# Optimization experiments

Measured on AMD Instinct MI355X. Metric: run time of the kernel, lower is better.

Reference implementation:

```python
import jax, jax.numpy as jnp
import numpy as np

B, N, F_IN, F_OUT = 1024, 16, 1024, 4096  # n_nodes=16 and n_heads=1 are structurally fixed by the module


def setup_inputs() -> dict:
    key = jax.random.key(0)
    ks = jax.random.split(key, 7)
    s1 = 1.0 / np.sqrt(F_IN)
    s2 = 1.0 / np.sqrt(F_IN * 16)
    return {
        "x": jax.random.normal(ks[0], (B, N, F_IN), jnp.float32),
        "matrix": jax.random.uniform(ks[1], (B, N, N), jnp.float32),
        "W1": jax.random.uniform(ks[2], (F_IN, F_IN), jnp.float32, -s1, s1),
        "b1": jax.random.uniform(ks[3], (F_IN,), jnp.float32, -s1, s1),
        "W_mlp": jax.random.uniform(ks[4], (F_OUT, F_IN * 16), jnp.float32, -s2, s2),
        "b_mlp": jax.random.uniform(ks[5], (F_OUT,), jnp.float32, -s2, s2),
        "a_param": jnp.float32(5.0),
    }


def _l2norm(v):
    # matches F.normalize(p=2, dim=-1, eps=1e-12)
    n = jnp.maximum(jnp.linalg.norm(v, axis=-1, keepdims=True), 1e-12)
    return v / n


def _forward(x, matrix, W1, b1, W_mlp, b_mlp, a_param):
    Bc, n, f = x.shape  # n_heads = 1, n_hidden = f
    wg = x @ W1.T + b1                                    # [B,n,f]
    gs = _l2norm(x)                                       # g_reshaped (H=1)
    gt = _l2norm(wg)                                      # g_transposed
    e = jnp.einsum('bik,bjk->bij', gs, gt)[..., None]     # [B,n,n,1] cosine scores
    eye = jnp.eye(n, dtype=x.dtype)[None, :, :, None]
    e = e * (1.0 + eye * a_param)                         # boost diagonal
    a_scores = e                                          # pre-softmax scores (used below)
    esm = jax.nn.softmax(e, axis=1)                       # softmax over dim=1
    m = matrix[..., None]                                 # [B,n,n,1]
    # MPUGAT message passing
    from_i = jnp.einsum('bitp,btkp->bikp', esm, m)        # [B,n,n,1]
    diag = jnp.einsum('bkkp->bkp', m)                     # diagonal of matrix
    from_j = esm * diag[:, None, :, :]                    # '...jkp,...kkp->...jkp'
    e2 = jnp.einsum('bikp,bjkp->bijp', from_i, from_j)    # [B,n,n,1]
    e2 = 0.5 * (e2 + jnp.transpose(e2, (0, 2, 1, 3)))
    # attention readout with PRE-softmax scores a_scores
    g = x.reshape(Bc, n, 1, f)                            # [B,n,H=1,f]
    attn = jnp.tanh(jnp.einsum('bjhf,bjih->bihf', g, a_scores))  # [B,n,1,f]
    out = attn.reshape(Bc, -1) @ W_mlp.T + b_mlp          # [B,F_OUT]
    out = jnp.broadcast_to(out[:, None, :], (Bc, 16, out.shape[-1]))  # repeat(1,16,1)
    return out, e2, m


def reference(x, matrix, W1, b1, W_mlp, b_mlp, a_param):
    return _forward(x, matrix, W1, b1, W_mlp, b_mlp, a_param)
```

## Files before the change

kernel.cpp:

```cpp
#include <hip/hip_runtime.h>
#include <math.h>

typedef short short8 __attribute__((ext_vector_type(8)));
typedef float f32x4 __attribute__((ext_vector_type(4)));
typedef unsigned short us4 __attribute__((ext_vector_type(4)));
typedef unsigned int u32x4 __attribute__((ext_vector_type(4)));
typedef unsigned short u16;
typedef unsigned int u32;

#define GAS __attribute__((address_space(1)))
#define LAS __attribute__((address_space(3)))

static __device__ __forceinline__ u16 f2bf(float f) {
    union { float f; u32 u; } v; v.f = f;
    u32 r = v.u + 0x7FFFu + ((v.u >> 16) & 1u);
    return (u16)(r >> 16);
}

static __device__ __forceinline__ u32 pk2(float a, float b) {
    return (u32)f2bf(a) | ((u32)f2bf(b) << 16);
}

static __device__ __forceinline__ u32 cvtpk(float lo, float hi) {
    u32 r;
    asm("v_cvt_pk_bf16_f32 %0, %1, %2" : "=v"(r) : "v"(lo), "v"(hi));
    return r;
}

static __device__ __forceinline__ float bf2f(u16 h) {
    union { u32 u; float f; } v; v.u = ((u32)h) << 16;
    return v.f;
}

static __device__ __forceinline__ float ftanh(float v) {
    float t = __expf(-2.0f * fabsf(v));
    float r = (1.0f - t) / (1.0f + t);
    return copysignf(r, v);
}

static __device__ __forceinline__ void gll16(const void* g, void* l) {
    __builtin_amdgcn_global_load_lds((const GAS void*)g, (LAS void*)l, 16, 0, 0);
}

__global__ __launch_bounds__(256) void k_cvt_x(const float* __restrict__ x,
                                               u16* __restrict__ xb,
                                               float* __restrict__ xinv,
                                               const float* __restrict__ W1,
                                               u16* __restrict__ w1b) {
    const int bid = blockIdx.x, t = threadIdx.x;
    if (bid >= 16384) {
        const size_t i = (size_t)(bid - 16384) * 256 + t;
        const f32x4 v = *(const f32x4*)(W1 + 4 * i);
        u32* dst = (u32*)(w1b + 4 * i);
        dst[0] = pk2(v.x, v.y); dst[1] = pk2(v.z, v.w);
        return;
    }
    const int row = bid;
    const f32x4 v = *(const f32x4*)(x + (size_t)row * 1024 + 4 * t);
    u32* dst = (u32*)(xb + (size_t)row * 1024 + 4 * t);
    dst[0] = pk2(v.x, v.y); dst[1] = pk2(v.z, v.w);
    float s = v.x * v.x + v.y * v.y + v.z * v.z + v.w * v.w;
#pragma unroll
    for (int off = 1; off < 64; off <<= 1) s += __shfl_xor(s, off, 64);
    __shared__ float red[4];
    if ((t & 63) == 0) red[t >> 6] = s;
    __syncthreads();
    if (t == 0)
        xinv[row] = 1.0f / fmaxf(sqrtf(red[0] + red[1] + red[2] + red[3]), 1e-12f);
}

#define MFMA16(a, b, c) __builtin_amdgcn_mfma_f32_16x16x32_bf16(a, b, c, 0, 0, 0)
#define SBAR() __builtin_amdgcn_s_barrier()
#define SCHED0() __builtin_amdgcn_sched_barrier(0)
#define PHFENCE() do { SBAR(); SCHED0(); } while (0)
#define VMW6 asm volatile("s_waitcnt vmcnt(6)" ::: "memory")
#define VMW4 asm volatile("s_waitcnt vmcnt(4)" ::: "memory")
#define VMW2 asm volatile("s_waitcnt vmcnt(2)" ::: "memory")
#define VMW0 asm volatile("s_waitcnt vmcnt(0)" ::: "memory")
#define VMW8L asm volatile("s_waitcnt vmcnt(8) lgkmcnt(0)" ::: "memory")
#define LGKML asm volatile("s_waitcnt lgkmcnt(0)" ::: "memory")
#define VMNOP do {} while (0)

#define DO_T1(I0, I1, I2, I3, W0, W1M, W2, W3)                                \
  do {                                                                        \
    short8 Af[4][2], Bf0[2][2], Bf1[2][2];                                    \
    _Pragma("unroll") for (int m = 0; m < 4; ++m) {                           \
      Af[m][0] = *(const short8*)(la + rpA[m] + sw0);                         \
      Af[m][1] = *(const short8*)(la + rpA[m] + sw1);                         \
    }                                                                         \
    _Pragma("unroll") for (int n = 0; n < 2; ++n) {                           \
      Bf0[n][0] = *(const short8*)(lb + rpB[n] + sw0);                        \
      Bf0[n][1] = *(const short8*)(lb + rpB[n] + sw1);                        \
    }                                                                         \
    if (I0) { gll16(AG + (saO00 + knxa), danext + ldst);                      \
              gll16(AG + (saO01 + knxa), danext + 4096 + ldst); }             \
    SBAR(); SCHED0();                                                         \
    __builtin_amdgcn_s_setprio(1);                                            \
    _Pragma("unroll") for (int k = 0; k < 2; ++k)                             \
      _Pragma("unroll") for (int m = 0; m < 4; ++m)                           \
        _Pragma("unroll") for (int n = 0; n < 2; ++n)                         \
          acc[m][n] = MFMA16(Af[m][k], Bf0[n][k], acc[m][n]);                 \
    __builtin_amdgcn_s_setprio(0); SCHED0(); W0; SBAR();                      \
    _Pragma("unroll") for (int n = 0; n < 2; ++n) {                           \
      Bf1[n][0] = *(const short8*)(lb + rpB[n + 2] + sw0);                    \
      Bf1[n][1] = *(const short8*)(lb + rpB[n + 2] + sw1);                    \
    }                                                                         \
    if (I1) { gll16(BG + (sbO10 + knxa), dbnext + 8192 + ldst);               \
              gll16(BG + (sbO11 + knxa), dbnext + 8192 + 4096 + ldst); }      \
    SBAR(); SCHED0();                                                         \
    __builtin_amdgcn_s_setprio(1);                                            \
    _Pragma("unroll") for (int k = 0; k < 2; ++k)                             \
      _Pragma("unroll") for (int m = 0; m < 4; ++m)                           \
        _Pragma("unroll") for (int n = 0; n < 2; ++n)                         \
          acc[m][n + 2] = MFMA16(Af[m][k], Bf1[n][k], acc[m][n + 2]);         \
    __builtin_amdgcn_s_setprio(0); SCHED0(); W1M; SBAR();                     \
    _Pragma("unroll") for (int m = 0; m < 4; ++m) {                           \
      Af[m][0] = *(const short8*)(la + rpA[m + 4] + sw0);                     \
      Af[m][1] = *(const short8*)(la + rpA[m + 4] + sw1);                     \
    }                                                                         \
    if (I2) { gll16(AG + (saO10 + knxa), danext + 8192 + ldst);               \
              gll16(AG + (saO11 + knxa), danext + 8192 + 4096 + ldst); }      \
    SBAR(); SCHED0();                                                         \
    __builtin_amdgcn_s_setprio(1);                                            \
    _Pragma("unroll") for (int k = 0; k < 2; ++k)                             \
      _Pragma("unroll") for (int m = 0; m < 4; ++m)                           \
        _Pragma("unroll") for (int n = 0; n < 2; ++n)                         \
          acc[m + 4][n] = MFMA16(Af[m][k], Bf0[n][k], acc[m + 4][n]);         \
    __builtin_amdgcn_s_setprio(0); SCHED0(); W2; SBAR();                      \
    if (I3) { gll16(BG + (sbO00 + knxb), lbw + ldst);                         \
              gll16(BG + (sbO01 + knxb), lbw + 4096 + ldst); }                \
    SBAR(); SCHED0();                                                         \
    __builtin_amdgcn_s_setprio(1);                                            \
    _Pragma("unroll") for (int k = 0; k < 2; ++k)                             \
      _Pragma("unroll") for (int m = 0; m < 4; ++m)                           \
        _Pragma("unroll") for (int n = 0; n < 2; ++n)                         \
          acc[m + 4][n + 2] = MFMA16(Af[m][k], Bf1[n][k], acc[m + 4][n + 2]); \
    __builtin_amdgcn_s_setprio(0); SCHED0(); W3; SBAR();                      \
  } while (0)

#define GEMM1_PROLOGUE()                                                      \
  do {                                                                        \
    gll16(AG + saO00, &LsA[0][0] + ldst);                                     \
    gll16(AG + saO01, &LsA[0][0] + 4096 + ldst);                              \
    gll16(BG + sbO00, &LsB[0][0] + ldst);                                     \
    gll16(BG + sbO01, &LsB[0][0] + 4096 + ldst);                              \
    gll16(BG + sbO10, &LsB[0][0] + 8192 + ldst);                              \
    gll16(BG + sbO11, &LsB[0][0] + 8192 + 4096 + ldst);                       \
    gll16(AG + saO10, &LsA[0][0] + 8192 + ldst);                              \
    gll16(AG + saO11, &LsA[0][0] + 8192 + 4096 + ldst);                       \
    gll16(BG + sbO00 + 64, &LsB[1][0] + ldst);                                \
    gll16(BG + sbO01 + 64, &LsB[1][0] + 4096 + ldst);                         \
    VMW6; SBAR();                                                             \
  } while (0)

#define GT2S(ISS, KNXA, KNXB, WAITX)                                          \
  do {                                                                        \
    short8 Af[4][2], Bf0[2][2], Bf1[2][2];                                    \
    _Pragma("unroll") for (int m = 0; m < 4; ++m) {                           \
      Af[m][0] = *(const short8*)(la + rpA[m] + sw0);                         \
      Af[m][1] = *(const short8*)(la + rpA[m] + sw1);                         \
    }                                                                         \
    _Pragma("unroll") for (int n = 0; n < 2; ++n) {                           \
      Bf0[n][0] = *(const short8*)(lb + rpB[n] + sw0);                        \
      Bf0[n][1] = *(const short8*)(lb + rpB[n] + sw1);                        \
    }                                                                         \
    if (ISS) { gll16(AG + (saO00 + (KNXA)), danext + ldst);                   \
               gll16(AG + (saO01 + (KNXA)), danext + 4096 + ldst); }          \
    PHFENCE();                                                                \
    __builtin_amdgcn_s_setprio(1);                                            \
    _Pragma("unroll") for (int k = 0; k < 2; ++k)                             \
      _Pragma("unroll") for (int m = 0; m < 4; ++m)                           \
        _Pragma("unroll") for (int n = 0; n < 2; ++n)                         \
          acc[m][n] = MFMA16(Af[m][k], Bf0[n][k], acc[m][n]);                 \
    __builtin_amdgcn_s_setprio(0); SCHED0(); SBAR();                          \
    _Pragma("unroll") for (int n = 0; n < 2; ++n) {                           \
      Bf1[n][0] = *(const short8*)(lb + rpB[n + 2] + sw0);                    \
      Bf1[n][1] = *(const short8*)(lb + rpB[n + 2] + sw1);                    \
    }                                                                         \
    if (ISS) { gll16(AG + (saO10 + (KNXA)), danext + 8192 + ldst);            \
               gll16(AG + (saO11 + (KNXA)), danext + 8192 + 4096 + ldst); }   \
    PHFENCE();                                                                \
    __builtin_amdgcn_s_setprio(1);                                            \
    _Pragma("unroll") for (int k = 0; k < 2; ++k)                             \
      _Pragma("unroll") for (int m = 0; m < 4; ++m)                           \
        _Pragma("unroll") for (int n = 0; n < 2; ++n)                         \
          acc[m][n + 2] = MFMA16(Af[m][k], Bf1[n][k], acc[m][n + 2]);         \
    __builtin_amdgcn_s_setprio(0); SCHED0(); SBAR();                          \
    _Pragma("unroll") for (int m = 0; m < 4; ++m) {                           \
      Af[m][0] = *(const short8*)(la + rpA[m + 4] + sw0);                     \
      Af[m][1] = *(const short8*)(la + rpA[m + 4] + sw1);                     \
    }                                                                         \
    PHFENCE();                                                                \
    __builtin_amdgcn_s_setprio(1);                                            \
    _Pragma("unroll") for (int k = 0; k < 2; ++k)                             \
      _Pragma("unroll") for (int m = 0; m < 4; ++m)                           \
        _Pragma("unroll") for (int n = 0; n < 2; ++n)                         \
          acc[m + 4][n] = MFMA16(Af[m][k], Bf0[n][k], acc[m + 4][n]);         \
    __builtin_amdgcn_s_setprio(0); SCHED0();                                  \
    if (ISS) {                                                                \
      _Pragma("unroll") for (int c = 0; c < 2; ++c) {                         \
        u32x4 wv;                                                             \
        wv.x = cvtpk(bn[2 * c].x, bn[2 * c].y);                               \
        wv.y = cvtpk(bn[2 * c].z, bn[2 * c].w);                               \
        wv.z = cvtpk(bn[2 * c + 1].x, bn[2 * c + 1].y);                       \
        wv.w = cvtpk(bn[2 * c + 1].z, bn[2 * c + 1].w);                       \
        *(u32x4*)(dbnext + c * 4096 + (tid << 3)) = wv;                       \
        bn[2 * c]     = *(const f32x4*)(BGf + bro[c] + (KNXB) + swsrc);       \
        bn[2 * c + 1] = *(const f32x4*)(BGf + bro[c] + (KNXB) + swsrc + 4);   \
      }                                                                       \
    }                                                                         \
    __builtin_amdgcn_s_setprio(1);                                            \
    _Pragma("unroll") for (int k = 0; k < 2; ++k)                             \
      _Pragma("unroll") for (int m = 0; m < 4; ++m)                           \
        _Pragma("unroll") for (int n = 0; n < 2; ++n)                         \
          acc[m + 4][n + 2] = MFMA16(Af[m][k], Bf1[n][k], acc[m + 4][n + 2]); \
    __builtin_amdgcn_s_setprio(0); SCHED0();                                  \
    if (ISS) {                                                                \
      _Pragma("unroll") for (int c = 2; c < 4; ++c) {                         \
        u32x4 wv;                                                             \
        wv.x = cvtpk(bn[2 * c].x, bn[2 * c].y);                               \
        wv.y = cvtpk(bn[2 * c].z, bn[2 * c].w);                               \
        wv.z = cvtpk(bn[2 * c + 1].x, bn[2 * c + 1].y);                       \
        wv.w = cvtpk(bn[2 * c + 1].z, bn[2 * c + 1].w);                       \
        *(u32x4*)(dbnext + c * 4096 + (tid << 3)) = wv;                       \
        bn[2 * c]     = *(const f32x4*)(BGf + bro[c] + (KNXB) + swsrc);       \
        bn[2 * c + 1] = *(const f32x4*)(BGf + bro[c] + (KNXB) + swsrc + 4);   \
      }                                                                       \
    }                                                                         \
    WAITX; SBAR();                                                            \
  } while (0)

__global__ __launch_bounds__(512, 2) void k_gemm1_8ph(const u16* __restrict__ AG,
                                                      const u16* __restrict__ BG,
                                                      const float* __restrict__ bias,
                                                      u16* __restrict__ C,
                                                      float* __restrict__ wgn2) {
    __shared__ __align__(16) u16 LsA[2][16384];
    __shared__ __align__(16) u16 LsB[2][16384];
    const int K = 1024, NT = 16;
    const int lin = blockIdx.x;
    const int w = (lin & 7) * 32 + (lin >> 3);
    const int n0 = (w & 3) * 256;
    const int m0 = (w >> 2) * 256;

    const int tid = threadIdx.x, wave = tid >> 6, lane = tid & 63;
    const int lr = lane & 15, kq = lane >> 4;
    const int wr = wave >> 2, wc = wave & 3;

    const int trow = tid >> 3;
    const u32 swsrc = (u32)(((tid & 7) ^ (trow & 7)) * 8);
    const u32 saO00 = (u32)(m0 + 0 + trow) * (u32)K + swsrc;
    const u32 saO01 = (u32)(m0 + 128 + trow) * (u32)K + swsrc;
    const u32 saO10 = (u32)(m0 + 64 + trow) * (u32)K + swsrc;
    const u32 saO11 = (u32)(m0 + 192 + trow) * (u32)K + swsrc;
    const int q0 = trow, q1 = 64 + trow;
    const u32 sbO00 = (u32)(n0 + (q0 >> 5) * 64 + (q0 & 31)) * (u32)K + swsrc;
    const u32 sbO01 = (u32)(n0 + (q1 >> 5) * 64 + (q1 & 31)) * (u32)K + swsrc;
    const u32 sbO10 = (u32)(n0 + (q0 >> 5) * 64 + 32 + (q0 & 31)) * (u32)K + swsrc;
    const u32 sbO11 = (u32)(n0 + (q1 >> 5) * 64 + 32 + (q1 & 31)) * (u32)K + swsrc;
    const u32 ldst = (u32)wave * 512;

    int rpA[8], rpB[4];
#pragma unroll
    for (int mf = 0; mf < 8; ++mf)
        rpA[mf] = ((mf >> 2) * 128 + wr * 64 + (mf & 3) * 16 + lr) << 6;
#pragma unroll
    for (int nf = 0; nf < 4; ++nf)
        rpB[nf] = ((nf >> 1) * 128 + wc * 32 + (nf & 1) * 16 + lr) << 6;
    const int sw0 = ((0 + kq) ^ (lr & 7)) * 8;
    const int sw1 = ((4 + kq) ^ (lr & 7)) * 8;

    f32x4 acc[8][4] = {};

    GEMM1_PROLOGUE();

    int cur = 0;
    for (int T = 0; T < NT - 2; ++T) {
        const u16* la = &LsA[cur][0];
        const u16* lb = &LsB[cur][0];
        u16* danext = &LsA[cur ^ 1][0];
        u16* dbnext = &LsB[cur ^ 1][0];
        u16* lbw = &LsB[cur][0];
        const u32 knxa = (u32)(T + 1) * 64;
        const u32 knxb = (u32)(T + 2) * 64;
        DO_T1(1, 1, 1, 1, VMW6, VMW6, VMW6, VMW6);
        cur ^= 1;
    }
    {
        const u16* la = &LsA[cur][0];
        const u16* lb = &LsB[cur][0];
        u16* danext = &LsA[cur ^ 1][0];
        u16* dbnext = &LsB[cur ^ 1][0];
        u16* lbw = &LsB[cur][0];
        const u32 knxa = (u32)(NT - 1) * 64, knxb = 0;
        (void)knxb;
        DO_T1(1, 1, 1, 0, VMW6, VMW6, VMW6, VMW4);
        cur ^= 1;
    }
    {
        const u16* la = &LsA[cur][0];
        const u16* lb = &LsB[cur][0];
        u16* danext = &LsA[cur ^ 1][0];
        u16* dbnext = &LsB[cur ^ 1][0];
        u16* lbw = &LsB[cur][0];
        const u32 knxa = 0, knxb = 0;
        (void)danext; (void)dbnext; (void)lbw; (void)knxa; (void)knxb;
        DO_T1(0, 0, 0, 0, VMW2, VMW0, VMNOP, VMNOP);
    }

    const int col0 = n0 + wc * 64;
    const int row0 = m0 + wr * 128;
    float bcol[4];
#pragma unroll
    for (int nf = 0; nf < 4; ++nf) bcol[nf] = bias[col0 + nf * 16 + lr];
#pragma unroll
    for (int mf = 0; mf < 8; ++mf) {
#pragma unroll
        for (int r = 0; r < 4; ++r) {
            const int row = row0 + mf * 16 + kq * 4 + r;
            float nrm = 0.f;
#pragma unroll
            for (int nf = 0; nf < 4; ++nf) {
                float v = acc[mf][nf][r] + bcol[nf];
                C[(size_t)row * 1024 + col0 + nf * 16 + lr] = f2bf(v);
                nrm += v * v;
            }
#pragma unroll
            for (int off = 1; off < 16; off <<= 1) nrm += __shfl_xor(nrm, off, 64);
            if (lr == 0) atomicAdd(&wgn2[row], nrm);
        }
    }
}

__global__ __launch_bounds__(512, 2) void k_gemm2_8ph(const u16* __restrict__ AG,
                                                      const float* __restrict__ BGf,
                                                      u16* __restrict__ part) {
    __shared__ __align__(16) u16 LsA[2][16384];
    __shared__ __align__(16) u16 LsB[2][16384];
    const int K = 16384, NT = 64;
    const int lin = blockIdx.x;
    const int w = (lin & 7) * 32 + (lin >> 3);
    const int m0 = (w & 3) * 256;
    const int z = (w >> 2) & 3;
    const int n0 = (w >> 4) * 256;
    const int kbeg = z * 4096;

    const int tid = threadIdx.x, wave = tid >> 6, lane = tid & 63;
    const int lr = lane & 15, kq = lane >> 4;
    const int wr = wave >> 2, wc = wave & 3;

    const int trow = tid >> 3;
    const u32 swsrc = (u32)(((tid & 7) ^ (trow & 7)) * 8);
    const u32 saO00 = (u32)(m0 + 0 + trow) * (u32)K + (u32)kbeg + swsrc;
    const u32 saO01 = (u32)(m0 + 128 + trow) * (u32)K + (u32)kbeg + swsrc;
    const u32 saO10 = (u32)(m0 + 64 + trow) * (u32)K + (u32)kbeg + swsrc;
    const u32 saO11 = (u32)(m0 + 192 + trow) * (u32)K + (u32)kbeg + swsrc;
    const int q0 = trow, q1 = 64 + trow;
    u32 bro[4];
    bro[0] = (u32)(n0 + (q0 >> 5) * 64 + (q0 & 31)) * 16384u + (u32)kbeg;
    bro[1] = (u32)(n0 + (q1 >> 5) * 64 + (q1 & 31)) * 16384u + (u32)kbeg;
    bro[2] = bro[0] + 32u * 16384u;
    bro[3] = bro[1] + 32u * 16384u;
    const u32 ldst = (u32)wave * 512;

    int rpA[8], rpB[4];
#pragma unroll
    for (int mf = 0; mf < 8; ++mf)
        rpA[mf] = ((mf >> 2) * 128 + wr * 64 + (mf & 3) * 16 + lr) << 6;
#pragma unroll
    for (int nf = 0; nf < 4; ++nf)
        rpB[nf] = ((nf >> 1) * 128 + wc * 32 + (nf & 1) * 16 + lr) << 6;
    const int sw0 = ((0 + kq) ^ (lr & 7)) * 8;
    const int sw1 = ((4 + kq) ^ (lr & 7)) * 8;

    f32x4 acc[8][4] = {};
    f32x4 bn[8];

    {
#pragma unroll
        for (int c = 0; c < 4; ++c) {
            bn[2 * c]     = *(const f32x4*)(BGf + bro[c] + swsrc);
            bn[2 * c + 1] = *(const f32x4*)(BGf + bro[c] + swsrc + 4);
        }
        gll16(AG + saO00, &LsA[0][0] + ldst);
        gll16(AG + saO01, &LsA[0][0] + 4096 + ldst);
        gll16(AG + saO10, &LsA[0][0] + 8192 + ldst);
        gll16(AG + saO11, &LsA[0][0] + 8192 + 4096 + ldst);
#pragma unroll
        for (int c = 0; c < 4; ++c) {
            u32x4 wv;
            wv.x = cvtpk(bn[2 * c].x, bn[2 * c].y);
            wv.y = cvtpk(bn[2 * c].z, bn[2 * c].w);
            wv.z = cvtpk(bn[2 * c + 1].x, bn[2 * c + 1].y);
            wv.w = cvtpk(bn[2 * c + 1].z, bn[2 * c + 1].w);
            *(u32x4*)(&LsB[0][0] + c * 4096 + (tid << 3)) = wv;
        }
        asm volatile("s_waitcnt vmcnt(0) lgkmcnt(0)" ::: "memory");
#pragma unroll
        for (int c = 0; c < 4; ++c) {
            bn[2 * c]     = *(const f32x4*)(BGf + bro[c] + 64 + swsrc);
            bn[2 * c + 1] = *(const f32x4*)(BGf + bro[c] + 64 + swsrc + 4);
        }
        SBAR();
    }

    int cur = 0;
    for (int T = 0; T < NT - 1; ++T) {
        const u16* la = &LsA[cur][0];
        const u16* lb = &LsB[cur][0];
        u16* danext = &LsA[cur ^ 1][0];
        u16* dbnext = &LsB[cur ^ 1][0];
        const u32 knxa = (u32)(T + 1) * 64;
        const u32 knxb = (T + 2 < NT) ? (u32)(T + 2) * 64 : 0u;
        GT2S(1, knxa, knxb, VMW8L);
        cur ^= 1;
    }
    {
        const u16* la = &LsA[cur][0];
        const u16* lb = &LsB[cur][0];
        u16* danext = &LsA[cur ^ 1][0];
        u16* dbnext = &LsB[cur ^ 1][0];
        (void)danext; (void)dbnext;
        GT2S(0, 0u, 0u, LGKML);
    }

    u16* po = part + (size_t)z * 4194304ull;
    const int col0 = n0 + wc * 64;
    const int row0 = m0 + wr * 128;
#pragma unroll
    for (int mf = 0; mf < 8; ++mf)
#pragma unroll
        for (int r = 0; r < 4; ++r) {
            const int row = row0 + mf * 16 + kq * 4 + r;
#pragma unroll
            for (int nf = 0; nf < 4; ++nf)
                po[(size_t)row * 4096 + col0 + nf * 16 + lr] = f2bf(acc[mf][nf][r]);
        }
}

__global__ __launch_bounds__(256) void k_batch_attn(const u16* xb,
                                                    const u16* __restrict__ wgb,
                                                    const float* __restrict__ xinv,
                                                    const float* __restrict__ wgn2,
                                                    const float* __restrict__ matrix,
                                                    const float* __restrict__ a_param,
                                                    float* __restrict__ e2_out,
                                                    float* __restrict__ m_out,
                                                    u16* attn_bf) {
    const int b = blockIdx.x, tid = threadIdx.x;
    const int wave = tid >> 6, lane = tid & 63;
    const int j = lane & 15, ig = (lane >> 4) * 4;

    __shared__ float qred[4][64][4];
    __shared__ float esm_l[16 * 17];
    __shared__ float fi_l[16 * 17];
    __shared__ float e2_l[16 * 17];
    __shared__ float m_l[256];
    __shared__ float as_l[256];
    __shared__ u16 xsh[16][256];

    {
        const size_t roff = (size_t)(b * 16 + j) * 1024 + (lane >> 4) * 8 + wave * 256;
        f32x4 acc0 = {}, acc1 = {};
#pragma unroll
        for (int kt = 0; kt < 256; kt += 64) {
            short8 xa0 = *(const short8*)(xb + roff + kt);
            short8 wa0 = *(const short8*)(wgb + roff + kt);
            short8 xa1 = *(const short8*)(xb + roff + kt + 32);
            short8 wa1 = *(const short8*)(wgb + roff + kt + 32);
            acc0 = __builtin_amdgcn_mfma_f32_16x16x32_bf16(xa0, wa0, acc0, 0, 0, 0);
            acc1 = __builtin_amdgcn_mfma_f32_16x16x32_bf16(xa1, wa1, acc1, 0, 0, 0);
        }
#pragma unroll
        for (int r = 0; r < 4; ++r) qred[wave][lane][r] = acc0[r] + acc1[r];
    }
    __syncthreads();

    if (tid < 64) {
        const int l = tid;
        const float inw = 1.0f / fmaxf(sqrtf(wgn2[b * 16 + j]), 1e-12f);
        const float boost = 1.0f + a_param[0];
        float e[4];
#pragma unroll
        for (int r = 0; r < 4; ++r) {
            const int i = ig + r;
            float v = (qred[0][l][r] + qred[1][l][r] + qred[2][l][r] + qred[3][l][r]) *
                      xinv[b * 16 + i] * inw;
            if (i == j) v *= boost;
            e[r] = v;
            as_l[i * 16 + j] = v;
        }
        float mx = fmaxf(fmaxf(e[0], e[1]), fmaxf(e[2], e[3]));
        mx = fmaxf(mx, __shfl_xor(mx, 16, 64));
        mx = fmaxf(mx, __shfl_xor(mx, 32, 64));
        float p[4], s = 0.f;
#pragma unroll
        for (int r = 0; r < 4; ++r) { p[r] = __expf(e[r] - mx); s += p[r]; }
        s += __shfl_xor(s, 16, 64);
        s += __shfl_xor(s, 32, 64);
        const float invs = 1.0f / s;
#pragma unroll
        for (int r = 0; r < 4; ++r) esm_l[(ig + r) * 17 + j] = p[r] * invs;
        const f32x4 mv = *(const f32x4*)(matrix + (size_t)b * 256 + 4 * l);
        *(f32x4*)(m_l + 4 * l) = mv;
        *(f32x4*)(m_out + (size_t)b * 256 + 4 * l) = mv;
    }
    __syncthreads();
    if (tid < 64) {
        float fi[4] = {0, 0, 0, 0};
#pragma unroll
        for (int t = 0; t < 16; ++t) {
            const float mk = m_l[t * 16 + j];
#pragma unroll
            for (int r = 0; r < 4; ++r) fi[r] += esm_l[(ig + r) * 17 + t] * mk;
        }
#pragma unroll
        for (int r = 0; r < 4; ++r) fi_l[(ig + r) * 17 + j] = fi[r];
    }
    __syncthreads();
    if (tid < 64) {
        float e2v[4] = {0, 0, 0, 0};
#pragma unroll
        for (int kk = 0; kk < 16; ++kk) {
            const float wgt = esm_l[j * 17 + kk] * m_l[kk * 16 + kk];
#pragma unroll
            for (int r = 0; r < 4; ++r) e2v[r] += fi_l[(ig + r) * 17 + kk] * wgt;
        }
#pragma unroll
        for (int r = 0; r < 4; ++r) e2_l[(ig + r) * 17 + j] = e2v[r];
    }
    __syncthreads();
    if (tid < 64) {
#pragma unroll
        for (int r = 0; r < 4; ++r) {
            const int i = ig + r;
            e2_out[(size_t)b * 256 + i * 16 + j] =
                0.5f * (e2_l[i * 17 + j] + e2_l[j * 17 + i]);
        }
    }

    const int srow = tid >> 4;
    const int scol = (tid & 15) * 16;
    for (int ch = 0; ch < 4; ++ch) {
        __syncthreads();
        const u16* src = xb + ((size_t)b * 16 + srow) * 1024 + ch * 256 + scol;
        *(short8*)&xsh[srow][scol] = *(const short8*)src;
        *(short8*)&xsh[srow][scol + 8] = *(const short8*)(src + 8);
        __syncthreads();
        float accv[16] = {};
#pragma unroll
        for (int jj = 0; jj < 16; ++jj) {
            const float xv = bf2f(xsh[jj][tid]);
#pragma unroll
            for (int i = 0; i < 16; ++i) accv[i] = fmaf(as_l[jj * 16 + i], xv, accv[i]);
        }
#pragma unroll
        for (int i = 0; i < 16; ++i)
            attn_bf[((size_t)b * 16 + i) * 1024 + ch * 256 + tid] = f2bf(ftanh(accv[i]));
    }
}

__global__ __launch_bounds__(256) void k_bcast(const u16* __restrict__ p,
                                               const float* __restrict__ bias,
                                               float* __restrict__ out) {
    const size_t i = (size_t)blockIdx.x * 256 + threadIdx.x;
    const int o4 = (int)(i & 1023);
    const int b = (int)(i >> 14);
    const size_t src = (size_t)b * 4096 + (size_t)o4 * 4;
    f32x4 r = *(const f32x4*)(bias + (size_t)o4 * 4);
#pragma unroll
    for (int z = 0; z < 4; ++z) {
        us4 v = *(const us4*)(p + (size_t)z * 4194304ull + src);
        r.x += bf2f(v.x); r.y += bf2f(v.y); r.z += bf2f(v.z); r.w += bf2f(v.w);
    }
    *(f32x4*)(out + i * 4) = r;
}

extern "C" void kernel_launch(void* const* d_in, const int* in_sizes, int n_in,
                              void* d_out, int out_size, void* d_ws, size_t ws_size,
                              hipStream_t stream) {
    const float* x      = (const float*)d_in[0];
    const float* matrix = (const float*)d_in[1];
    const float* W1     = (const float*)d_in[2];
    const float* b1     = (const float*)d_in[3];
    const float* W_mlp  = (const float*)d_in[4];
    const float* b_mlp  = (const float*)d_in[5];
    const float* a_par  = (const float*)d_in[6];
    float* out = (float*)d_out;

    char* ws = (char*)d_ws;
    size_t off = 0;
    auto alloc = [&](size_t bytes) {
        char* p = ws + off;
        off += (bytes + 255) & ~(size_t)255;
        return p;
    };
    u16*   x_bf  = (u16*)alloc(16384ull * 1024 * 2);
    u16*   wg_bf = (u16*)alloc(16384ull * 1024 * 2);
    u16*   w1_bf = (u16*)alloc(1024ull * 1024 * 2);
    float* xinv  = (float*)alloc(16384ull * 4);
    float* wgn2  = (float*)alloc(16384ull * 4);
    u16*   attn_bf = x_bf;
    u16*   part    = wg_bf;
    float* e2_out = out + 67108864ull;
    float* m_out  = out + 67371008ull;

    hipMemsetAsync(wgn2, 0, 16384 * 4, stream);
    k_cvt_x<<<17408, 256, 0, stream>>>(x, x_bf, xinv, W1, w1_bf);
    k_gemm1_8ph<<<256, 512, 0, stream>>>(x_bf, w1_bf, b1, wg_bf, wgn2);
    k_batch_attn<<<1024, 256, 0, stream>>>(x_bf, wg_bf, xinv, wgn2, matrix, a_par,
                                           e2_out, m_out, attn_bf);
    k_gemm2_8ph<<<256, 512, 0, stream>>>(attn_bf, W_mlp, part);
    k_bcast<<<65536, 256, 0, stream>>>(part, b_mlp, out);
}
```

Measured before the change: 334.2 us.

## Drop intra-iteration barriers in split-K GEMM mainloop and peel final iterations

Replaces the GT2S phase macro with GT3, which issues all four next-tile A global-to-LDS loads at the start of the iteration. It reads all B fragments up front and runs the MFMA phases without the barriers between them, so only the end-of-iteration barrier remains. The last prefetching iteration is peeled so it converts and stores the already-loaded B tile without issuing further B reads, and waits with vmcnt(0) before the final compute-only iteration. This cuts barrier stalls and lets waves drift apart, at the cost of more registers live at once and weaker control over how loads and MFMAs interleave.

```diff
diff --git a/kernel.cpp b/kernel.cpp
--- a/kernel.cpp
+++ b/kernel.cpp
@@ -72,12 +72,12 @@
 #define MFMA16(a, b, c) __builtin_amdgcn_mfma_f32_16x16x32_bf16(a, b, c, 0, 0, 0)
 #define SBAR() __builtin_amdgcn_s_barrier()
 #define SCHED0() __builtin_amdgcn_sched_barrier(0)
-#define PHFENCE() do { SBAR(); SCHED0(); } while (0)
 #define VMW6 asm volatile("s_waitcnt vmcnt(6)" ::: "memory")
 #define VMW4 asm volatile("s_waitcnt vmcnt(4)" ::: "memory")
 #define VMW2 asm volatile("s_waitcnt vmcnt(2)" ::: "memory")
 #define VMW0 asm volatile("s_waitcnt vmcnt(0)" ::: "memory")
 #define VMW8L asm volatile("s_waitcnt vmcnt(8) lgkmcnt(0)" ::: "memory")
+#define VMW0L asm volatile("s_waitcnt vmcnt(0) lgkmcnt(0)" ::: "memory")
 #define LGKML asm volatile("s_waitcnt lgkmcnt(0)" ::: "memory")
 #define VMNOP do {} while (0)
 
@@ -153,9 +153,15 @@
     VMW6; SBAR();                                                             \
   } while (0)
 
-#define GT2S(ISS, KNXA, KNXB, WAITX)                                          \
+#define GT3(ISSA, ISSC, ISSB, KNXA, KNXB, WEND)                               \
   do {                                                                        \
     short8 Af[4][2], Bf0[2][2], Bf1[2][2];                                    \
+    if (ISSA) {                                                               \
+      gll16(AG + (saO00 + (KNXA)), danext + ldst);                            \
+      gll16(AG + (saO01 + (KNXA)), danext + 4096 + ldst);                     \
+      gll16(AG + (saO10 + (KNXA)), danext + 8192 + ldst);                     \
+      gll16(AG + (saO11 + (KNXA)), danext + 8192 + 4096 + ldst);              \
+    }                                                                         \
     _Pragma("unroll") for (int m = 0; m < 4; ++m) {                           \
       Af[m][0] = *(const short8*)(la + rpA[m] + sw0);                         \
       Af[m][1] = *(const short8*)(la + rpA[m] + sw1);                         \
@@ -163,41 +169,30 @@
     _Pragma("unroll") for (int n = 0; n < 2; ++n) {                           \
       Bf0[n][0] = *(const short8*)(lb + rpB[n] + sw0);                        \
       Bf0[n][1] = *(const short8*)(lb + rpB[n] + sw1);                        \
-    }                                                                         \
-    if (ISS) { gll16(AG + (saO00 + (KNXA)), danext + ldst);                   \
-               gll16(AG + (saO01 + (KNXA)), danext + 4096 + ldst); }          \
-    PHFENCE();                                                                \
-    __builtin_amdgcn_s_setprio(1);                                            \
-    _Pragma("unroll") for (int k = 0; k < 2; ++k)                             \
-      _Pragma("unroll") for (int m = 0; m < 4; ++m)                           \
-        _Pragma("unroll") for (int n = 0; n < 2; ++n)                         \
-          acc[m][n] = MFMA16(Af[m][k], Bf0[n][k], acc[m][n]);                 \
-    __builtin_amdgcn_s_setprio(0); SCHED0(); SBAR();                          \
-    _Pragma("unroll") for (int n = 0; n < 2; ++n) {                           \
       Bf1[n][0] = *(const short8*)(lb + rpB[n + 2] + sw0);                    \
       Bf1[n][1] = *(const short8*)(lb + rpB[n + 2] + sw1);                    \
     }                                                                         \
-    if (ISS) { gll16(AG + (saO10 + (KNXA)), danext + 8192 + ldst);            \
-               gll16(AG + (saO11 + (KNXA)), danext + 8192 + 4096 + ldst); }   \
-    PHFENCE();                                                                \
     __builtin_amdgcn_s_setprio(1);                                            \
     _Pragma("unroll") for (int k = 0; k < 2; ++k)                             \
       _Pragma("unroll") for (int m = 0; m < 4; ++m)                           \
         _Pragma("unroll") for (int n = 0; n < 2; ++n)                         \
+          acc[m][n] = MFMA16(Af[m][k], Bf0[n][k], acc[m][n]);                 \
+    _Pragma("unroll") for (int k = 0; k < 2; ++k)                             \
+      _Pragma("unroll") for (int m = 0; m < 4; ++m)                           \
+        _Pragma("unroll") for (int n = 0; n < 2; ++n)                         \
           acc[m][n + 2] = MFMA16(Af[m][k], Bf1[n][k], acc[m][n + 2]);         \
-    __builtin_amdgcn_s_setprio(0); SCHED0(); SBAR();                          \
+    __builtin_amdgcn_s_setprio(0);                                            \
     _Pragma("unroll") for (int m = 0; m < 4; ++m) {                           \
       Af[m][0] = *(const short8*)(la + rpA[m + 4] + sw0);                     \
       Af[m][1] = *(const short8*)(la + rpA[m + 4] + sw1);                     \
     }                                                                         \
-    PHFENCE();                                                                \
     __builtin_amdgcn_s_setprio(1);                                            \
     _Pragma("unroll") for (int k = 0; k < 2; ++k)                             \
       _Pragma("unroll") for (int m = 0; m < 4; ++m)                           \
         _Pragma("unroll") for (int n = 0; n < 2; ++n)                         \
           acc[m + 4][n] = MFMA16(Af[m][k], Bf0[n][k], acc[m + 4][n]);         \
-    __builtin_amdgcn_s_setprio(0); SCHED0();                                  \
-    if (ISS) {                                                                \
+    __builtin_amdgcn_s_setprio(0);                                            \
+    if (ISSC) {                                                               \
       _Pragma("unroll") for (int c = 0; c < 2; ++c) {                         \
         u32x4 wv;                                                             \
         wv.x = cvtpk(bn[2 * c].x, bn[2 * c].y);                               \
@@ -205,8 +200,10 @@
         wv.z = cvtpk(bn[2 * c + 1].x, bn[2 * c + 1].y);                       \
         wv.w = cvtpk(bn[2 * c + 1].z, bn[2 * c + 1].w);                       \
         *(u32x4*)(dbnext + c * 4096 + (tid << 3)) = wv;                       \
-        bn[2 * c]     = *(const f32x4*)(BGf + bro[c] + (KNXB) + swsrc);       \
-        bn[2 * c + 1] = *(const f32x4*)(BGf + bro[c] + (KNXB) + swsrc + 4);   \
+        if (ISSB) {                                                           \
+          bn[2 * c]     = *(const f32x4*)(BGf + bro[c] + (KNXB) + swsrc);     \
+          bn[2 * c + 1] = *(const f32x4*)(BGf + bro[c] + (KNXB) + swsrc + 4); \
+        }                                                                     \
       }                                                                       \
     }                                                                         \
     __builtin_amdgcn_s_setprio(1);                                            \
@@ -214,8 +211,8 @@
       _Pragma("unroll") for (int m = 0; m < 4; ++m)                           \
         _Pragma("unroll") for (int n = 0; n < 2; ++n)                         \
           acc[m + 4][n + 2] = MFMA16(Af[m][k], Bf1[n][k], acc[m + 4][n + 2]); \
-    __builtin_amdgcn_s_setprio(0); SCHED0();                                  \
-    if (ISS) {                                                                \
+    __builtin_amdgcn_s_setprio(0);                                            \
+    if (ISSC) {                                                               \
       _Pragma("unroll") for (int c = 2; c < 4; ++c) {                         \
         u32x4 wv;                                                             \
         wv.x = cvtpk(bn[2 * c].x, bn[2 * c].y);                               \
@@ -223,11 +220,13 @@
         wv.z = cvtpk(bn[2 * c + 1].x, bn[2 * c + 1].y);                       \
         wv.w = cvtpk(bn[2 * c + 1].z, bn[2 * c + 1].w);                       \
         *(u32x4*)(dbnext + c * 4096 + (tid << 3)) = wv;                       \
-        bn[2 * c]     = *(const f32x4*)(BGf + bro[c] + (KNXB) + swsrc);       \
-        bn[2 * c + 1] = *(const f32x4*)(BGf + bro[c] + (KNXB) + swsrc + 4);   \
+        if (ISSB) {                                                           \
+          bn[2 * c]     = *(const f32x4*)(BGf + bro[c] + (KNXB) + swsrc);     \
+          bn[2 * c + 1] = *(const f32x4*)(BGf + bro[c] + (KNXB) + swsrc + 4); \
+        }                                                                     \
       }                                                                       \
     }                                                                         \
-    WAITX; SBAR();                                                            \
+    SCHED0(); WEND; SBAR();                                                   \
   } while (0)
 
 __global__ __launch_bounds__(512, 2) void k_gemm1_8ph(const u16* __restrict__ AG,
@@ -377,15 +376,15 @@
     f32x4 bn[8];
 
     {
-#pragma unroll
-        for (int c = 0; c < 4; ++c) {
-            bn[2 * c]     = *(const f32x4*)(BGf + bro[c] + swsrc);
-            bn[2 * c + 1] = *(const f32x4*)(BGf + bro[c] + swsrc + 4);
-        }
         gll16(AG + saO00, &LsA[0][0] + ldst);
         gll16(AG + saO01, &LsA[0][0] + 4096 + ldst);
         gll16(AG + saO10, &LsA[0][0] + 8192 + ldst);
         gll16(AG + saO11, &LsA[0][0] + 8192 + 4096 + ldst);
+#pragma unroll
+        for (int c = 0; c < 4; ++c) {
+            bn[2 * c]     = *(const f32x4*)(BGf + bro[c] + swsrc);
+            bn[2 * c + 1] = *(const f32x4*)(BGf + bro[c] + swsrc + 4);
+        }
 #pragma unroll
         for (int c = 0; c < 4; ++c) {
             u32x4 wv;
@@ -405,14 +404,24 @@
     }
 
     int cur = 0;
-    for (int T = 0; T < NT - 1; ++T) {
+    for (int T = 0; T < NT - 2; ++T) {
         const u16* la = &LsA[cur][0];
         const u16* lb = &LsB[cur][0];
         u16* danext = &LsA[cur ^ 1][0];
         u16* dbnext = &LsB[cur ^ 1][0];
         const u32 knxa = (u32)(T + 1) * 64;
-        const u32 knxb = (T + 2 < NT) ? (u32)(T + 2) * 64 : 0u;
-        GT2S(1, knxa, knxb, VMW8L);
+        const u32 knxb = (u32)(T + 2) * 64;
+        GT3(1, 1, 1, knxa, knxb, VMW8L);
+        cur ^= 1;
+    }
+    {
+        const u16* la = &LsA[cur][0];
+        const u16* lb = &LsB[cur][0];
+        u16* danext = &LsA[cur ^ 1][0];
+        u16* dbnext = &LsB[cur ^ 1][0];
+        const u32 knxa = 63u * 64, knxb = 0;
+        (void)knxb;
+        GT3(1, 1, 0, knxa, 0u, VMW0L);
         cur ^= 1;
     }
     {
@@ -421,7 +430,7 @@
         u16* danext = &LsA[cur ^ 1][0];
         u16* dbnext = &LsB[cur ^ 1][0];
         (void)danext; (void)dbnext;
-        GT2S(0, 0u, 0u, LGKML);
+        GT3(0, 0, 0, 0u, 0u, VMNOP);
     }
 
     u16* po = part + (size_t)z * 4194304ull;
```

Result: faster. 318.4 us (-4.7%).
